# Kernel tuning notes

Measured on AMD Instinct MI355X. Metric: run time of the kernel, lower is better.

Reference implementation:

```python
import jax, jax.numpy as jnp
import numpy as np
import itertools

F = 3          # num_sparse_features
C = 256        # num_categories
D = 64         # embedding_dim
H = 1024       # hidden_units
ND = 13        # num_dense_features
B = 16384      # batch
COMBOS = [c for r in range(2, F + 1) for c in itertools.combinations(range(F), r)]
WIDE_DIM = C * F + sum(C ** len(c) for c in COMBOS) + ND
DEEP_IN = F * D + ND


def setup_inputs() -> dict:
    key = jax.random.key(0)
    ks = jax.random.split(key, 12)
    sparse_inputs = jax.random.randint(ks[0], (B, F), 0, C, dtype=jnp.int32)
    dense_inputs = jax.random.normal(ks[1], (B, ND), dtype=jnp.float32)
    wide_w = jax.random.normal(ks[2], (WIDE_DIM,), dtype=jnp.float32) * 0.01
    wide_b = jax.random.normal(ks[3], (1,), dtype=jnp.float32) * 0.01
    emb = jax.random.normal(ks[4], (F, C, D), dtype=jnp.float32) * 0.05
    W1 = jax.random.normal(ks[5], (H, DEEP_IN), dtype=jnp.float32) / np.sqrt(DEEP_IN).astype(np.float32)
    b1 = jnp.zeros((H,), jnp.float32)
    W2 = jax.random.normal(ks[6], (H, H), dtype=jnp.float32) / np.sqrt(H).astype(np.float32)
    b2 = jnp.zeros((H,), jnp.float32)
    W3 = jax.random.normal(ks[7], (1, H), dtype=jnp.float32) / np.sqrt(H).astype(np.float32)
    b3 = jnp.zeros((1,), jnp.float32)
    return {"sparse_inputs": sparse_inputs, "dense_inputs": dense_inputs,
            "wide_w": wide_w, "wide_b": wide_b, "emb": emb,
            "W1": W1, "b1": b1, "W2": W2, "b2": b2, "W3": W3, "b3": b3}


def reference(sparse_inputs, dense_inputs, wide_w, wide_b, emb, W1, b1, W2, b2, W3, b3):
    # Wide path: one_hot(x) @ W.T  ==  gather of W columns at the hot indices.
    wide = wide_b[0]  # scalar, broadcasts to [B]
    for i in range(F):  # per-feature one-hot block, width C each
        wide = wide + wide_w[i * C + sparse_inputs[:, i]]
    off = F * C
    for combo in COMBOS:  # cross-feature one-hot blocks, width C**len(combo)
        cross = sparse_inputs[:, combo[0]]
        for j in combo[1:]:
            # faithful to source: multiplies by num_sparse_features (F), not C
            cross = cross * F + sparse_inputs[:, j]
        wide = wide + wide_w[off + cross]
        off += C ** len(combo)
    wide = wide + dense_inputs @ wide_w[off:off + ND]  # dense tail of wide linear
    wide = wide[:, None]  # [B, 1]

    # Deep path: per-feature embedding lookup -> concat -> 3-layer MLP
    embedded = jnp.concatenate([emb[i][sparse_inputs[:, i]] for i in range(F)], axis=1)  # [B, F*D]
    deep_x = jnp.concatenate([embedded, dense_inputs], axis=1)  # [B, DEEP_IN]
    h = jax.nn.relu(deep_x @ W1.T + b1)
    h = jax.nn.relu(h @ W2.T + b2)
    deep = h @ W3.T + b3  # [B, 1]

    return jax.nn.sigmoid(wide + deep)
```

## Files before the change

### kernel.cpp

```cpp
#include <hip/hip_runtime.h>
#include <stdint.h>


#define BATCH 16384
#define HDIM 1024
#define K1 256
#define DEEP_IN 205

typedef short bf16x8 __attribute__((ext_vector_type(8)));
typedef float f32x4 __attribute__((ext_vector_type(4)));
typedef uint16_t u16x8 __attribute__((ext_vector_type(8)));
typedef uint16_t u16x4 __attribute__((ext_vector_type(4)));

__device__ __forceinline__ uint16_t f2bf(float f) {
    uint32_t x;
    __builtin_memcpy(&x, &f, 4);
    uint32_t r = (x + 0x7fffu + ((x >> 16) & 1u)) >> 16;
    return (uint16_t)r;
}

__device__ __forceinline__ void async_ld16(const uint16_t* g, uint16_t* l) {
    __builtin_amdgcn_global_load_lds(
        (const __attribute__((address_space(1))) uint32_t*)g,
        (__attribute__((address_space(3))) uint32_t*)l, 16, 0, 0);
}

__global__ __launch_bounds__(256) void prep_kernel(
    const int* __restrict__ sp, const float* __restrict__ dense,
    const float* __restrict__ emb, const float* __restrict__ W1,
    const float* __restrict__ W2, const float* __restrict__ ww,
    const float* __restrict__ wb, const float* __restrict__ b3,
    uint16_t* __restrict__ dx, uint16_t* __restrict__ W1b,
    uint16_t* __restrict__ W2b, float* __restrict__ wide)
{
    const int bid = blockIdx.x;
    const int tid = threadIdx.x;
    if (bid < 2048) {
        int idx = bid * 256 + tid;
        int b = idx >> 5, c0 = (idx & 31) * 8;
        u16x8 o;
        if (c0 < 192) {
            int f = c0 >> 6, cc = c0 & 63;
            int s = sp[b * 3 + f];
            const float* e = emb + (size_t)(((f << 8) + s) * 64 + cc);
            float4 v0 = *(const float4*)e;
            float4 v1 = *(const float4*)(e + 4);
            o[0] = f2bf(v0.x); o[1] = f2bf(v0.y); o[2] = f2bf(v0.z); o[3] = f2bf(v0.w);
            o[4] = f2bf(v1.x); o[5] = f2bf(v1.y); o[6] = f2bf(v1.z); o[7] = f2bf(v1.w);
        } else {
#pragma unroll
            for (int t = 0; t < 8; t++) {
                int c = c0 + t;
                o[t] = (c < DEEP_IN) ? f2bf(dense[b * 13 + (c - 192)])
                                     : (uint16_t)0;
            }
        }
        *(u16x8*)(dx + (size_t)b * K1 + c0) = o;
    } else if (bid < 2176) {
        int idx = (bid - 2048) * 256 + tid;
        int n = idx >> 5, c0 = (idx & 31) * 8;
        u16x8 o;
#pragma unroll
        for (int t = 0; t < 8; t++) {
            int c = c0 + t;
            o[t] = (c < DEEP_IN) ? f2bf(W1[n * DEEP_IN + c]) : (uint16_t)0;
        }
        *(u16x8*)(W1b + (size_t)n * K1 + c0) = o;
    } else if (bid < 2688) {
        int k = (bid - 2176) * 256 + tid;
        const float* src = W2 + (size_t)k * 8;
        float4 v0 = *(const float4*)src;
        float4 v1 = *(const float4*)(src + 4);
        u16x8 o;
        o[0] = f2bf(v0.x); o[1] = f2bf(v0.y); o[2] = f2bf(v0.z); o[3] = f2bf(v0.w);
        o[4] = f2bf(v1.x); o[5] = f2bf(v1.y); o[6] = f2bf(v1.z); o[7] = f2bf(v1.w);
        *(u16x8*)(W2b + (size_t)k * 8) = o;
    } else {
        int b = (bid - 2688) * 256 + tid;
        int s0 = sp[b * 3], s1 = sp[b * 3 + 1], s2 = sp[b * 3 + 2];
        float w = wb[0] + b3[0];
        w += ww[s0] + ww[256 + s1] + ww[512 + s2];
        w += ww[768    + s0 * 3 + s1];
        w += ww[66304  + s0 * 3 + s2];
        w += ww[131840 + s1 * 3 + s2];
        w += ww[197376 + (s0 * 3 + s1) * 3 + s2];
        const float* wd = ww + 16974592;
        float acc2 = 0.f;
#pragma unroll
        for (int j = 0; j < 13; j++) acc2 += dense[b * 13 + j] * wd[j];
        wide[b] = w + acc2;
    }
}

#define BAR8() do { asm volatile("" ::: "memory");                             \
    __builtin_amdgcn_s_barrier();                                              \
    asm volatile("" ::: "memory"); } while (0)
#define VM4() asm volatile("s_waitcnt vmcnt(4)" ::: "memory")

#define STG8(grow, regoff, h, kt) do {                                         \
    const uint16_t* g_ = (grow) + (size_t)((h) * 128) * (size_t)K + (kt);      \
    async_ld16(g_, &lds[(regoff) + (h) * 8192 + wave * 512]);                  \
    async_ld16(g_ + (size_t)64 * (size_t)K,                                    \
               &lds[(regoff) + (h) * 8192 + 4096 + wave * 512]);               \
} while (0)

#define LDA8(base, msub) do {                                                  \
    _Pragma("unroll") for (int mt = 0; mt < 4; mt++) {                         \
        int ro_ = (base) + ((msub) * 64 + mt * 16) * 64;                       \
        af[mt][0] = *(const bf16x8*)&lds[ro_ + kc0];                           \
        af[mt][1] = *(const bf16x8*)&lds[ro_ + kc1];                           \
    } } while (0)

#define LDB8(dst, base, nsub) do {                                             \
    _Pragma("unroll") for (int nt = 0; nt < 2; nt++) {                         \
        int ro_ = (base) + ((nsub) * 32 + nt * 16) * 64;                       \
        dst[nt][0] = *(const bf16x8*)&lds[ro_ + kc0];                          \
        dst[nt][1] = *(const bf16x8*)&lds[ro_ + kc1];                          \
    } } while (0)

#define MM8(msub, nsub, BF) do {                                               \
    __builtin_amdgcn_s_setprio(1);                                             \
    _Pragma("unroll") for (int mt = 0; mt < 4; mt++)                           \
    _Pragma("unroll") for (int nt = 0; nt < 2; nt++) {                         \
        acc[(msub)*4+mt][(nsub)*2+nt] = __builtin_amdgcn_mfma_f32_16x16x32_bf16( \
            af[mt][0], BF[nt][0], acc[(msub)*4+mt][(nsub)*2+nt], 0, 0, 0);     \
        acc[(msub)*4+mt][(nsub)*2+nt] = __builtin_amdgcn_mfma_f32_16x16x32_bf16( \
            af[mt][1], BF[nt][1], acc[(msub)*4+mt][(nsub)*2+nt], 0, 0, 0);     \
    }                                                                          \
    __builtin_amdgcn_s_setprio(0); } while (0)

#define GEMM8_DECLS()                                                          \
    const int tid = threadIdx.x;                                               \
    const int lane = tid & 63, wave = tid >> 6;                                \
    const int wm = wave >> 2, wn = wave & 3;                                   \
    const int id = blockIdx.x;                                                 \
    const int wg = (id & 7) * 32 + (id >> 3);                                  \
    const int by = wg >> 2, bx = wg & 3;                                       \
    const int bm = by * 256, bn = bx * 256;                                    \
    const int lam = lane & 15, lad = lane >> 4;                                \
    const int sw = (lane & 7) << 4;                                            \
    const int kc0 = ((lad * 16) ^ sw) >> 1;                                    \
    const int kc1 = ((64 + lad * 16) ^ sw) >> 1;                               \
    const int aBE = wm * 8192 + lam * 64;                                      \
    const int aBO = aBE + 16384;                                               \
    const int bBE = 32768 + (wn >> 1) * 8192 + ((wn & 1) * 64 + lam) * 64;     \
    const int bBO = bBE + 16384;                                               \
    const int trow = tid >> 3;                                                 \
    const int csel = ((tid & 7) ^ (trow & 7)) << 3;

#define GEMM8_MAIN()                                                           \
    f32x4 acc[8][4];                                                           \
    _Pragma("unroll") for (int i = 0; i < 8; i++)                              \
        _Pragma("unroll") for (int j = 0; j < 4; j++) acc[i][j] = (f32x4)0.f;  \
    bf16x8 af[4][2], bf0[2][2], bf1[2][2];                                     \
    const int NT = K >> 6;                                                     \
    const int NI = K >> 7;                                                     \
    STG8(aRow, 0, 0, 0);     STG8(aRow, 0, 1, 0);                              \
    STG8(bRow, 32768, 0, 0); STG8(bRow, 32768, 1, 0);                          \
    STG8(bRow, 49152, 0, 64); STG8(bRow, 49152, 1, 64);                        \
    VM4();                                                                     \
    BAR8();                                                                    \
    for (int it = 0; it < NI; ++it) {                                          \
        const int k1 = (2 * it + 1) * 64;                                      \
        const int t2 = 2 * it + 2, t3 = 2 * it + 3;                            \
        const int k2 = (t2 < NT ? t2 : 0) * 64;                                \
        const int k3 = (t3 < NT ? t3 : 0) * 64;                                \
        LDA8(aBE, 0); LDB8(bf0, bBE, 0); STG8(aRow, 16384, 0, k1);             \
        BAR8(); MM8(0, 0, bf0); BAR8();                                        \
        LDB8(bf1, bBE, 1); STG8(aRow, 16384, 1, k1);                           \
        BAR8(); MM8(0, 1, bf1); BAR8();                                        \
        LDA8(aBE, 1); STG8(bRow, 32768, 0, k2);                                \
        BAR8(); MM8(1, 1, bf1); BAR8();                                        \
        STG8(bRow, 32768, 1, k2);                                              \
        BAR8(); MM8(1, 0, bf0); VM4(); BAR8();                                 \
        LDA8(aBO, 0); LDB8(bf0, bBO, 0); STG8(aRow, 0, 0, k2);                 \
        BAR8(); MM8(0, 0, bf0); BAR8();                                        \
        LDB8(bf1, bBO, 1); STG8(aRow, 0, 1, k2);                               \
        BAR8(); MM8(0, 1, bf1); BAR8();                                        \
        LDA8(aBO, 1); STG8(bRow, 49152, 0, k3);                                \
        BAR8(); MM8(1, 1, bf1); BAR8();                                        \
        STG8(bRow, 49152, 1, k3);                                              \
        BAR8(); MM8(1, 0, bf0); VM4(); BAR8();                                 \
    }

__global__ __launch_bounds__(512, 2) void gemm1_8(
    const uint16_t* __restrict__ A, const uint16_t* __restrict__ Bw,
    const float* __restrict__ bias, uint16_t* __restrict__ C,
    int M, int N, int K)
{
    __shared__ __align__(16) uint16_t lds[65536];
    GEMM8_DECLS()
    const uint16_t* aRow = A + (size_t)(bm + trow) * K + csel;
    const int prow = 4 * (trow & 15) + (trow >> 4);
    const uint16_t* bRow = Bw + (size_t)(bn + prow) * K + csel;
    GEMM8_MAIN()

    float bv[4];
#pragma unroll
    for (int jn = 0; jn < 4; jn++) bv[jn] = bias[bn + wn * 64 + 4 * lam + jn];
#pragma unroll
    for (int im = 0; im < 8; im++) {
#pragma unroll
        for (int r = 0; r < 4; r++) {
            int m = bm + wm * 128 + im * 16 + lad * 4 + r;
            u16x4 o;
#pragma unroll
            for (int jn = 0; jn < 4; jn++)
                o[jn] = f2bf(fmaxf(acc[im][jn][r] + bv[jn], 0.f));
            *(u16x4*)&C[(size_t)m * N + bn + wn * 64 + 4 * lam] = o;
        }
    }
}

__global__ __launch_bounds__(512, 2) void gemm_fused8(
    const uint16_t* __restrict__ A, const uint16_t* __restrict__ Bw,
    const float* __restrict__ bias, const float* __restrict__ W3,
    float* __restrict__ outacc, int M, int N, int K)
{
    __shared__ __align__(16) uint16_t lds[65536];
    GEMM8_DECLS()
    const uint16_t* aRow = A + (size_t)(bm + trow) * K + csel;
    const uint16_t* bRow = Bw + (size_t)(bn + trow) * K + csel;
    GEMM8_MAIN()

    float bv[4], w3v[4];
#pragma unroll
    for (int jn = 0; jn < 4; jn++) {
        int n = bn + wn * 64 + jn * 16 + lam;
        bv[jn] = bias[n];
        w3v[jn] = W3[n];
    }
#pragma unroll
    for (int im = 0; im < 8; im++) {
#pragma unroll
        for (int r = 0; r < 4; r++) {
            float pt = 0.f;
#pragma unroll
            for (int jn = 0; jn < 4; jn++)
                pt += fmaxf(acc[im][jn][r] + bv[jn], 0.f) * w3v[jn];
            pt += __shfl_xor(pt, 1);
            pt += __shfl_xor(pt, 2);
            pt += __shfl_xor(pt, 4);
            pt += __shfl_xor(pt, 8);
            if (lam == 0) {
                int m = bm + wm * 128 + im * 16 + lad * 4 + r;
                atomicAdd(&outacc[m], pt);
            }
        }
    }
}

__global__ __launch_bounds__(256) void sigmoid_kernel(
    const float* __restrict__ outacc, float* __restrict__ out)
{
    int b = blockIdx.x * 256 + threadIdx.x;
    out[b] = 1.f / (1.f + __expf(-outacc[b]));
}

extern "C" void kernel_launch(void* const* d_in, const int* in_sizes, int n_in,
                              void* d_out, int out_size, void* d_ws, size_t ws_size,
                              hipStream_t stream) {
    const int*   sp    = (const int*)d_in[0];
    const float* dense = (const float*)d_in[1];
    const float* ww    = (const float*)d_in[2];
    const float* wb    = (const float*)d_in[3];
    const float* emb   = (const float*)d_in[4];
    const float* W1    = (const float*)d_in[5];
    const float* b1    = (const float*)d_in[6];
    const float* W2    = (const float*)d_in[7];
    const float* b2    = (const float*)d_in[8];
    const float* W3    = (const float*)d_in[9];
    const float* b3    = (const float*)d_in[10];
    float* out = (float*)d_out;

    char* ws = (char*)d_ws;
    float*    wide = (float*)ws;
    uint16_t* dxp  = (uint16_t*)(ws + 65536);
    uint16_t* W1b  = (uint16_t*)(ws + 8454144);
    uint16_t* W2b  = (uint16_t*)(ws + 8978432);
    uint16_t* h1   = (uint16_t*)(ws + 11075584);

    prep_kernel<<<2752, 256, 0, stream>>>(
        sp, dense, emb, W1, W2, ww, wb, b3, dxp, W1b, W2b, wide);
    gemm1_8<<<256, 512, 0, stream>>>(
        dxp, W1b, b1, h1, BATCH, HDIM, K1);
    gemm_fused8<<<256, 512, 0, stream>>>(
        h1, W2b, b2, W3, wide, BATCH, HDIM, HDIM);
    sigmoid_kernel<<<BATCH / 256, 256, 0, stream>>>(wide, out);
}
```

Baseline: 160.7 us.

## Fuse embedding gather into first GEMM's A-tile loads

Instead of materialising a gathered bf16 deep-input matrix [B,256] in the prep kernel, the prep kernel now only converts the embedding table to bf16 and writes a small padded dense tail. The first GEMM reads the sparse indices per row, packs them into registers, and issues its async global-to-LDS loads directly from the bf16 embedding table rows (for K<192) or from the dense tail. This removes an 8 MB write plus its re-read. In exchange the A loads become gathers, and each GEMM block adds index loads with a full vmcnt(0) wait before the main loop.

```diff
diff --git a/kernel.cpp b/kernel.cpp
--- a/kernel.cpp
+++ b/kernel.cpp
@@ -30,34 +30,33 @@
     const float* __restrict__ emb, const float* __restrict__ W1,
     const float* __restrict__ W2, const float* __restrict__ ww,
     const float* __restrict__ wb, const float* __restrict__ b3,
-    uint16_t* __restrict__ dx, uint16_t* __restrict__ W1b,
-    uint16_t* __restrict__ W2b, float* __restrict__ wide)
+    uint16_t* __restrict__ embb, uint16_t* __restrict__ dtail,
+    uint16_t* __restrict__ W1b, uint16_t* __restrict__ W2b,
+    float* __restrict__ wide)
 {
     const int bid = blockIdx.x;
     const int tid = threadIdx.x;
-    if (bid < 2048) {
-        int idx = bid * 256 + tid;
-        int b = idx >> 5, c0 = (idx & 31) * 8;
+    if (bid < 24) {
+        int k = bid * 256 + tid;
+        const float* src = emb + (size_t)k * 8;
+        float4 v0 = *(const float4*)src;
+        float4 v1 = *(const float4*)(src + 4);
         u16x8 o;
-        if (c0 < 192) {
-            int f = c0 >> 6, cc = c0 & 63;
-            int s = sp[b * 3 + f];
-            const float* e = emb + (size_t)(((f << 8) + s) * 64 + cc);
-            float4 v0 = *(const float4*)e;
-            float4 v1 = *(const float4*)(e + 4);
-            o[0] = f2bf(v0.x); o[1] = f2bf(v0.y); o[2] = f2bf(v0.z); o[3] = f2bf(v0.w);
-            o[4] = f2bf(v1.x); o[5] = f2bf(v1.y); o[6] = f2bf(v1.z); o[7] = f2bf(v1.w);
-        } else {
-#pragma unroll
-            for (int t = 0; t < 8; t++) {
-                int c = c0 + t;
-                o[t] = (c < DEEP_IN) ? f2bf(dense[b * 13 + (c - 192)])
-                                     : (uint16_t)0;
-            }
+        o[0] = f2bf(v0.x); o[1] = f2bf(v0.y); o[2] = f2bf(v0.z); o[3] = f2bf(v0.w);
+        o[4] = f2bf(v1.x); o[5] = f2bf(v1.y); o[6] = f2bf(v1.z); o[7] = f2bf(v1.w);
+        *(u16x8*)(embb + (size_t)k * 8) = o;
+    } else if (bid < 536) {
+        int idx = (bid - 24) * 256 + tid;
+        int b = idx >> 3, c0 = (idx & 7) * 8;
+        u16x8 o;
+#pragma unroll
+        for (int t = 0; t < 8; t++) {
+            int c = c0 + t;
+            o[t] = (c < 13) ? f2bf(dense[b * 13 + c]) : (uint16_t)0;
         }
-        *(u16x8*)(dx + (size_t)b * K1 + c0) = o;
-    } else if (bid < 2176) {
-        int idx = (bid - 2048) * 256 + tid;
+        *(u16x8*)(dtail + (size_t)b * 64 + c0) = o;
+    } else if (bid < 664) {
+        int idx = (bid - 536) * 256 + tid;
         int n = idx >> 5, c0 = (idx & 31) * 8;
         u16x8 o;
 #pragma unroll
@@ -66,8 +65,8 @@
             o[t] = (c < DEEP_IN) ? f2bf(W1[n * DEEP_IN + c]) : (uint16_t)0;
         }
         *(u16x8*)(W1b + (size_t)n * K1 + c0) = o;
-    } else if (bid < 2688) {
-        int k = (bid - 2176) * 256 + tid;
+    } else if (bid < 1176) {
+        int k = (bid - 664) * 256 + tid;
         const float* src = W2 + (size_t)k * 8;
         float4 v0 = *(const float4*)src;
         float4 v1 = *(const float4*)(src + 4);
@@ -76,7 +75,7 @@
         o[4] = f2bf(v1.x); o[5] = f2bf(v1.y); o[6] = f2bf(v1.z); o[7] = f2bf(v1.w);
         *(u16x8*)(W2b + (size_t)k * 8) = o;
     } else {
-        int b = (bid - 2688) * 256 + tid;
+        int b = (bid - 1176) * 256 + tid;
         int s0 = sp[b * 3], s1 = sp[b * 3 + 1], s2 = sp[b * 3 + 2];
         float w = wb[0] + b3[0];
         w += ww[s0] + ww[256 + s1] + ww[512 + s2];
@@ -96,13 +95,7 @@
     __builtin_amdgcn_s_barrier();                                              \
     asm volatile("" ::: "memory"); } while (0)
 #define VM4() asm volatile("s_waitcnt vmcnt(4)" ::: "memory")
-
-#define STG8(grow, regoff, h, kt) do {                                         \
-    const uint16_t* g_ = (grow) + (size_t)((h) * 128) * (size_t)K + (kt);      \
-    async_ld16(g_, &lds[(regoff) + (h) * 8192 + wave * 512]);                  \
-    async_ld16(g_ + (size_t)64 * (size_t)K,                                    \
-               &lds[(regoff) + (h) * 8192 + 4096 + wave * 512]);               \
-} while (0)
+#define VM0() asm volatile("s_waitcnt vmcnt(0)" ::: "memory")
 
 #define LDA8(base, msub) do {                                                  \
     _Pragma("unroll") for (int mt = 0; mt < 4; mt++) {                         \
@@ -155,9 +148,9 @@
     bf16x8 af[4][2], bf0[2][2], bf1[2][2];                                     \
     const int NT = K >> 6;                                                     \
     const int NI = K >> 7;                                                     \
-    STG8(aRow, 0, 0, 0);     STG8(aRow, 0, 1, 0);                              \
-    STG8(bRow, 32768, 0, 0); STG8(bRow, 32768, 1, 0);                          \
-    STG8(bRow, 49152, 0, 64); STG8(bRow, 49152, 1, 64);                        \
+    STG8A(0, 0, 0);     STG8A(0, 1, 0);                                        \
+    STG8B(32768, 0, 0); STG8B(32768, 1, 0);                                    \
+    STG8B(49152, 0, 64); STG8B(49152, 1, 64);                                  \
     VM4();                                                                     \
     BAR8();                                                                    \
     for (int it = 0; it < NI; ++it) {                                          \
@@ -165,34 +158,67 @@
         const int t2 = 2 * it + 2, t3 = 2 * it + 3;                            \
         const int k2 = (t2 < NT ? t2 : 0) * 64;                                \
         const int k3 = (t3 < NT ? t3 : 0) * 64;                                \
-        LDA8(aBE, 0); LDB8(bf0, bBE, 0); STG8(aRow, 16384, 0, k1);             \
+        LDA8(aBE, 0); LDB8(bf0, bBE, 0); STG8A(16384, 0, k1);                  \
         BAR8(); MM8(0, 0, bf0); BAR8();                                        \
-        LDB8(bf1, bBE, 1); STG8(aRow, 16384, 1, k1);                           \
+        LDB8(bf1, bBE, 1); STG8A(16384, 1, k1);                                \
         BAR8(); MM8(0, 1, bf1); BAR8();                                        \
-        LDA8(aBE, 1); STG8(bRow, 32768, 0, k2);                                \
+        LDA8(aBE, 1); STG8B(32768, 0, k2);                                     \
         BAR8(); MM8(1, 1, bf1); BAR8();                                        \
-        STG8(bRow, 32768, 1, k2);                                              \
+        STG8B(32768, 1, k2);                                                   \
         BAR8(); MM8(1, 0, bf0); VM4(); BAR8();                                 \
-        LDA8(aBO, 0); LDB8(bf0, bBO, 0); STG8(aRow, 0, 0, k2);                 \
+        LDA8(aBO, 0); LDB8(bf0, bBO, 0); STG8A(0, 0, k2);                      \
         BAR8(); MM8(0, 0, bf0); BAR8();                                        \
-        LDB8(bf1, bBO, 1); STG8(aRow, 0, 1, k2);                               \
+        LDB8(bf1, bBO, 1); STG8A(0, 1, k2);                                    \
         BAR8(); MM8(0, 1, bf1); BAR8();                                        \
-        LDA8(aBO, 1); STG8(bRow, 49152, 0, k3);                                \
+        LDA8(aBO, 1); STG8B(49152, 0, k3);                                     \
         BAR8(); MM8(1, 1, bf1); BAR8();                                        \
-        STG8(bRow, 49152, 1, k3);                                              \
+        STG8B(49152, 1, k3);                                                   \
         BAR8(); MM8(1, 0, bf0); VM4(); BAR8();                                 \
     }
 
+#define ASRC1(pkv, h2, kt) ((kt) < 192                                         \
+    ? (embb + (((kt) >> 6) << 14)                                              \
+            + ((int)(((pkv) >> (((kt) >> 6) << 3)) & 255u) << 6) + csel)       \
+    : (dtail + (size_t)(b0 + (h2) * 64) * 64 + csel))
+
+#define STG8A(regoff, h, kt) do {                                              \
+    async_ld16(ASRC1(PK##h##_0, 2*(h), kt),                                    \
+               &lds[(regoff) + (h) * 8192 + wave * 512]);                      \
+    async_ld16(ASRC1(PK##h##_1, 2*(h)+1, kt),                                  \
+               &lds[(regoff) + (h) * 8192 + 4096 + wave * 512]);               \
+} while (0)
+
+#define STG8B(regoff, h, kt) do {                                              \
+    const uint16_t* g_ = bRow + (size_t)((h) * 128) * (size_t)K + (kt);        \
+    async_ld16(g_, &lds[(regoff) + (h) * 8192 + wave * 512]);                  \
+    async_ld16(g_ + (size_t)64 * (size_t)K,                                    \
+               &lds[(regoff) + (h) * 8192 + 4096 + wave * 512]);               \
+} while (0)
+
 __global__ __launch_bounds__(512, 2) void gemm1_8(
-    const uint16_t* __restrict__ A, const uint16_t* __restrict__ Bw,
-    const float* __restrict__ bias, uint16_t* __restrict__ C,
-    int M, int N, int K)
+    const int* __restrict__ sp, const uint16_t* __restrict__ embb,
+    const uint16_t* __restrict__ dtail, const uint16_t* __restrict__ Bw,
+    const float* __restrict__ bias, uint16_t* __restrict__ C)
 {
     __shared__ __align__(16) uint16_t lds[65536];
     GEMM8_DECLS()
-    const uint16_t* aRow = A + (size_t)(bm + trow) * K + csel;
+    const int K = K1;
+    const int b0 = bm + trow;
+    const uint32_t PK0_0 = (uint32_t)sp[(b0      ) * 3] |
+                           ((uint32_t)sp[(b0      ) * 3 + 1] << 8) |
+                           ((uint32_t)sp[(b0      ) * 3 + 2] << 16);
+    const uint32_t PK0_1 = (uint32_t)sp[(b0 +  64) * 3] |
+                           ((uint32_t)sp[(b0 +  64) * 3 + 1] << 8) |
+                           ((uint32_t)sp[(b0 +  64) * 3 + 2] << 16);
+    const uint32_t PK1_0 = (uint32_t)sp[(b0 + 128) * 3] |
+                           ((uint32_t)sp[(b0 + 128) * 3 + 1] << 8) |
+                           ((uint32_t)sp[(b0 + 128) * 3 + 2] << 16);
+    const uint32_t PK1_1 = (uint32_t)sp[(b0 + 192) * 3] |
+                           ((uint32_t)sp[(b0 + 192) * 3 + 1] << 8) |
+                           ((uint32_t)sp[(b0 + 192) * 3 + 2] << 16);
     const int prow = 4 * (trow & 15) + (trow >> 4);
     const uint16_t* bRow = Bw + (size_t)(bn + prow) * K + csel;
+    VM0();
     GEMM8_MAIN()
 
     float bv[4];
@@ -207,10 +233,27 @@
 #pragma unroll
             for (int jn = 0; jn < 4; jn++)
                 o[jn] = f2bf(fmaxf(acc[im][jn][r] + bv[jn], 0.f));
-            *(u16x4*)&C[(size_t)m * N + bn + wn * 64 + 4 * lam] = o;
+            *(u16x4*)&C[(size_t)m * HDIM + bn + wn * 64 + 4 * lam] = o;
         }
     }
 }
+
+#undef STG8A
+#undef STG8B
+
+#define STG8A(regoff, h, kt) do {                                              \
+    const uint16_t* g_ = aRow + (size_t)((h) * 128) * (size_t)K + (kt);        \
+    async_ld16(g_, &lds[(regoff) + (h) * 8192 + wave * 512]);                  \
+    async_ld16(g_ + (size_t)64 * (size_t)K,                                    \
+               &lds[(regoff) + (h) * 8192 + 4096 + wave * 512]);               \
+} while (0)
+
+#define STG8B(regoff, h, kt) do {                                              \
+    const uint16_t* g_ = bRow + (size_t)((h) * 128) * (size_t)K + (kt);        \
+    async_ld16(g_, &lds[(regoff) + (h) * 8192 + wave * 512]);                  \
+    async_ld16(g_ + (size_t)64 * (size_t)K,                                    \
+               &lds[(regoff) + (h) * 8192 + 4096 + wave * 512]);               \
+} while (0)
 
 __global__ __launch_bounds__(512, 2) void gemm_fused8(
     const uint16_t* __restrict__ A, const uint16_t* __restrict__ Bw,
@@ -249,6 +292,9 @@
         }
     }
 }
+
+#undef STG8A
+#undef STG8B
 
 __global__ __launch_bounds__(256) void sigmoid_kernel(
     const float* __restrict__ outacc, float* __restrict__ out)
@@ -274,16 +320,17 @@
     float* out = (float*)d_out;
 
     char* ws = (char*)d_ws;
-    float*    wide = (float*)ws;
-    uint16_t* dxp  = (uint16_t*)(ws + 65536);
-    uint16_t* W1b  = (uint16_t*)(ws + 8454144);
-    uint16_t* W2b  = (uint16_t*)(ws + 8978432);
-    uint16_t* h1   = (uint16_t*)(ws + 11075584);
-
-    prep_kernel<<<2752, 256, 0, stream>>>(
-        sp, dense, emb, W1, W2, ww, wb, b3, dxp, W1b, W2b, wide);
+    float*    wide  = (float*)ws;
+    uint16_t* embb  = (uint16_t*)(ws + 65536);
+    uint16_t* dtail = (uint16_t*)(ws + 163840);
+    uint16_t* W1b   = (uint16_t*)(ws + 2260992);
+    uint16_t* W2b   = (uint16_t*)(ws + 2785280);
+    uint16_t* h1    = (uint16_t*)(ws + 4882432);
+
+    prep_kernel<<<1240, 256, 0, stream>>>(
+        sp, dense, emb, W1, W2, ww, wb, b3, embb, dtail, W1b, W2b, wide);
     gemm1_8<<<256, 512, 0, stream>>>(
-        dxp, W1b, b1, h1, BATCH, HDIM, K1);
+        sp, embb, dtail, W1b, b1, h1);
     gemm_fused8<<<256, 512, 0, stream>>>(
         h1, W2b, b2, W3, wide, BATCH, HDIM, HDIM);
     sigmoid_kernel<<<BATCH / 256, 256, 0, stream>>>(wide, out);
```

Measured after the change: 159.2 us, median of 2. About the same (-0.9%).
